# Kernel optimization log

Hardware: AMD Instinct MI355X
Metric: run time of the kernel (lower is better)

The kernel has to match this reference:

```python
import jax, jax.numpy as jnp
import numpy as np

N_HEADS = 16
N_KV_HEADS = 8
DIM = 2048
HEAD_DIM = DIM // N_HEADS  # 128
N_REP = N_HEADS // N_KV_HEADS


def _rope(t, cos, sin):
    # t: [B, S, H, D]; cos/sin: [S, D//2]
    t2 = t.reshape(*t.shape[:-1], -1, 2)  # [B,S,H,D/2,2]
    p1, p2 = t2[..., 0], t2[..., 1]
    c = cos[None, :, None, :]
    s = sin[None, :, None, :]
    r1 = p1 * c - p2 * s
    r2 = p1 * s + p2 * c
    return jnp.stack((r1, r2), axis=-1).reshape(t.shape)


def setup_inputs() -> dict:
    key = jax.random.key(0)
    ks = jax.random.split(key, 7)
    B, S = 2, 2048
    x = jax.random.normal(ks[0], (B, S, DIM), dtype=jnp.float32)
    freqs_cos = jax.random.normal(ks[1], (S, HEAD_DIM // 2), dtype=jnp.float32)
    freqs_sin = jax.random.normal(ks[2], (S, HEAD_DIM // 2), dtype=jnp.float32)
    sc = 1.0 / np.sqrt(DIM)
    wq = jax.random.normal(ks[3], (DIM, N_HEADS * HEAD_DIM), dtype=jnp.float32) * sc
    wk = jax.random.normal(ks[4], (DIM, N_KV_HEADS * HEAD_DIM), dtype=jnp.float32) * sc
    wv = jax.random.normal(ks[5], (DIM, N_KV_HEADS * HEAD_DIM), dtype=jnp.float32) * sc
    wo = jax.random.normal(ks[6], (N_HEADS * HEAD_DIM, DIM), dtype=jnp.float32) * sc
    return {"x": x, "freqs_cos": freqs_cos, "freqs_sin": freqs_sin,
            "wq": wq, "wk": wk, "wv": wv, "wo": wo}


def reference(x, freqs_cos, freqs_sin, wq, wk, wv, wo):
    B, S, _ = x.shape
    xq = (x @ wq).reshape(B, S, N_HEADS, HEAD_DIM)
    xk = (x @ wk).reshape(B, S, N_KV_HEADS, HEAD_DIM)
    xv = (x @ wv).reshape(B, S, N_KV_HEADS, HEAD_DIM)
    xq = _rope(xq, freqs_cos, freqs_sin)
    xk = _rope(xk, freqs_cos, freqs_sin)
    # GQA repeat_kv: [B,S,Hkv,D] -> [B,S,Hkv*n_rep,D]
    xk = jnp.repeat(xk, N_REP, axis=2)
    xv = jnp.repeat(xv, N_REP, axis=2)
    q = xq.transpose(0, 2, 1, 3)  # [B,H,S,D]
    k = xk.transpose(0, 2, 1, 3)
    v = xv.transpose(0, 2, 1, 3)
    scale = 1.0 / np.sqrt(HEAD_DIM)
    scores = jnp.einsum('bhqd,bhkd->bhqk', q, k) * scale
    causal = jnp.tril(jnp.ones((S, S), dtype=bool))
    scores = jnp.where(causal[None, None], scores, -jnp.inf)
    probs = jax.nn.softmax(scores.astype(jnp.float32), axis=-1).astype(q.dtype)
    out = jnp.einsum('bhqk,bhkd->bhqd', probs, v)
    out = out.transpose(0, 2, 1, 3).reshape(B, S, N_HEADS * HEAD_DIM)
    return out @ wo
```

## Files before the change

kernel.cpp:

```cpp
#include <hip/hip_runtime.h>
#include <cstdint>
#include <cstddef>

#define S_LEN 2048
#define DIM_   2048
#define NH   16
#define NKV  8
#define HD   128

typedef __attribute__((ext_vector_type(8))) __bf16 bf16x8;
typedef __attribute__((ext_vector_type(4))) float  f32x4;

typedef const __attribute__((address_space(1))) void* gptr_t;
typedef __attribute__((address_space(3))) void*       sptr_t;

static __device__ __forceinline__ float bf2f(unsigned short u) {
  union { unsigned int i; float f; } v; v.i = ((unsigned int)u) << 16; return v.f;
}
static __device__ __forceinline__ unsigned short f2bf(float f) {
  union { float f; unsigned int i; } v; v.f = f;
  unsigned int u = v.i;
  unsigned int r = (u + 0x7FFFu + ((u >> 16) & 1u)) >> 16;
  return (unsigned short)r;
}
static __device__ __forceinline__ unsigned int cvt_pk_bf16(float a, float b) {
  unsigned int r;
  asm volatile("v_cvt_pk_bf16_f32 %0, %1, %2" : "=v"(r) : "v"(a), "v"(b));
  return r;
}

#define QSCALE 0.12751744f
#define RESC_THR 11.542f

__global__ void k_prep(const float* __restrict__ x, unsigned short* __restrict__ xb,
                       const float* __restrict__ wq, const float* __restrict__ wk,
                       const float* __restrict__ wv, const float* __restrict__ wo,
                       unsigned short* __restrict__ wqkvT, unsigned short* __restrict__ woT) {
  int bid = blockIdx.x;
  if (bid < 8192) {
    int i = bid * 256 + threadIdx.x;
    float4 v = ((const float4*)x)[i];
    ushort4 o; o.x = f2bf(v.x); o.y = f2bf(v.y); o.z = f2bf(v.z); o.w = f2bf(v.w);
    ((ushort4*)xb)[i] = o;
    return;
  }
  bid -= 8192;
  const float* src; unsigned short* dst; int N, ntx;
  if (bid < 1024)      { src = wq; dst = wqkvT;                       N = 2048; ntx = 32; }
  else if (bid < 1536) { bid -= 1024; src = wk; dst = wqkvT + (size_t)2048 * 2048; N = 1024; ntx = 16; }
  else if (bid < 2048) { bid -= 1536; src = wv; dst = wqkvT + (size_t)3072 * 2048; N = 1024; ntx = 16; }
  else                 { bid -= 2048; src = wo; dst = woT;            N = 2048; ntx = 32; }
  const int K = 2048;
  __shared__ float tile[64][65];
  int lx = threadIdx.x & 15, ly = threadIdx.x >> 4;
  int r0 = (bid / ntx) * 64, c0 = (bid % ntx) * 64;
  #pragma unroll
  for (int i = 0; i < 4; i++) {
    int row = ly + 16 * i;
    float4 v = *(const float4*)(&src[(size_t)(r0 + row) * N + c0 + lx * 4]);
    tile[row][lx * 4 + 0] = v.x; tile[row][lx * 4 + 1] = v.y;
    tile[row][lx * 4 + 2] = v.z; tile[row][lx * 4 + 3] = v.w;
  }
  __syncthreads();
  #pragma unroll
  for (int i = 0; i < 4; i++) {
    int nrow = ly + 16 * i;
    ushort4 o;
    o.x = f2bf(tile[lx * 4 + 0][nrow]); o.y = f2bf(tile[lx * 4 + 1][nrow]);
    o.z = f2bf(tile[lx * 4 + 2][nrow]); o.w = f2bf(tile[lx * 4 + 3][nrow]);
    *(ushort4*)(&dst[(size_t)(c0 + nrow) * K + r0 + lx * 4]) = o;
  }
}

template<int MODE, int BM_, int TPB>
__global__ __launch_bounds__(TPB, 2) void k_gemm_bt(
    const unsigned short* __restrict__ A, const unsigned short* __restrict__ BT,
    void* __restrict__ C, int N, int K,
    const float* __restrict__ fc, const float* __restrict__ fs,
    unsigned short* __restrict__ kb, unsigned short* __restrict__ vb) {
  constexpr int NI = (BM_ == 64) ? 2 : 4;
  constexpr int AR = (BM_ * 64) / (TPB * 8);
  constexpr int BR = (128 * 64) / (TPB * 8);
  __shared__ __align__(16) unsigned short Asm[BM_ * 64];
  __shared__ __align__(16) unsigned short Bsm[128 * 64];
  const int t = threadIdx.x;
  const int lane = t & 63, w = t >> 6;
  const int wm = (BM_ == 64) ? 0 : (w >> 1) * 64;
  const int wn = (BM_ == 64) ? w * 32 : (w & 1) * 64;
  const int col = lane & 15, quad = lane >> 4;
  const int m0 = blockIdx.y * BM_, n0 = blockIdx.x * 128;

  f32x4 acc[4][NI];
  #pragma unroll
  for (int i = 0; i < 4; i++)
    #pragma unroll
    for (int j = 0; j < NI; j++) acc[i][j] = (f32x4){0.f, 0.f, 0.f, 0.f};

  for (int kk = 0; kk < K; kk += 64) {
    #pragma unroll
    for (int r = 0; r < AR; ++r) {
      int c = t + r * TPB;
      int c0 = (t & ~63) + r * TPB;
      int row = c >> 3;
      int kcs = (c & 7) ^ (row & 7);
      const unsigned short* gA = A + (size_t)(m0 + row) * K + kk + kcs * 8;
      __builtin_amdgcn_global_load_lds((gptr_t)gA, (sptr_t)(&Asm[c0 * 8]), 16, 0, 0);
    }
    #pragma unroll
    for (int r = 0; r < BR; ++r) {
      int c = t + r * TPB;
      int c0 = (t & ~63) + r * TPB;
      int row = c >> 3;
      int kcs = (c & 7) ^ (row & 7);
      const unsigned short* gB = BT + (size_t)(n0 + row) * K + kk + kcs * 8;
      __builtin_amdgcn_global_load_lds((gptr_t)gB, (sptr_t)(&Bsm[c0 * 8]), 16, 0, 0);
    }
    __syncthreads();
    #pragma unroll
    for (int kc2 = 0; kc2 < 2; kc2++) {
      bf16x8 af[4], bf[NI];
      #pragma unroll
      for (int mi = 0; mi < 4; mi++) {
        int rowA = wm + mi * 16 + col;
        af[mi] = *(const bf16x8*)(&Asm[rowA * 64 + (((kc2 * 4 + quad) ^ (col & 7)) * 8)]);
      }
      #pragma unroll
      for (int ni = 0; ni < NI; ni++) {
        int rowB = wn + ni * 16 + col;
        bf[ni] = *(const bf16x8*)(&Bsm[rowB * 64 + (((kc2 * 4 + quad) ^ (col & 7)) * 8)]);
      }
      #pragma unroll
      for (int mi = 0; mi < 4; mi++)
        #pragma unroll
        for (int ni = 0; ni < NI; ni++)
          acc[mi][ni] = __builtin_amdgcn_mfma_f32_16x16x32_bf16(af[mi], bf[ni], acc[mi][ni], 0, 0, 0);
    }
    __syncthreads();
  }

  #pragma unroll
  for (int mi = 0; mi < 4; mi++) {
    int row_base = m0 + wm + mi * 16 + quad * 4;
    #pragma unroll
    for (int ni = 0; ni < NI; ni++) {
      int col_g = n0 + wn + ni * 16 + col;
      if (MODE == 1) {
        float* O = (float*)C;
        #pragma unroll
        for (int r = 0; r < 4; r++) O[(size_t)(row_base + r) * N + col_g] = acc[mi][ni][r];
      } else {
        int region = col_g >> 10;
        if (region < 3) {
          int ri = (col_g & 127) >> 1;
          float sgn = (col_g & 1) ? 1.f : -1.f;
          unsigned short* qO = (unsigned short*)C;
          #pragma unroll
          for (int r = 0; r < 4; r++) {
            int row = row_base + r;
            int s = row & (S_LEN - 1);
            float cv = fc[s * 64 + ri], sv = fs[s * 64 + ri];
            float val = acc[mi][ni][r];
            float other = __shfl_xor(val, 1);
            float res = val * cv + sgn * other * sv;
            if (region < 2) qO[(size_t)row * 2048 + col_g] = f2bf(res * QSCALE);
            else            kb[(size_t)row * 1024 + (col_g - 2048)] = f2bf(res);
          }
        } else {
          int n_local = col_g - 3072;
          int b = row_base >> 11, s = row_base & (S_LEN - 1);
          int kvh = n_local >> 7, d = n_local & (HD - 1);
          ushort4 o4;
          o4.x = f2bf(acc[mi][ni][0]); o4.y = f2bf(acc[mi][ni][1]);
          o4.z = f2bf(acc[mi][ni][2]); o4.w = f2bf(acc[mi][ni][3]);
          *(ushort4*)(&vb[((size_t)((b * NKV + kvh) * HD + d)) * S_LEN + s]) = o4;
        }
      }
    }
  }
}

#define KLD 136
#define VLD 72
#define PLD 72
__global__ __launch_bounds__(512, 2) void k_attn(
    const unsigned short* __restrict__ q, const unsigned short* __restrict__ k,
    const unsigned short* __restrict__ vT, unsigned short* __restrict__ ao) {
  __shared__ __align__(16) unsigned short Ksm[64 * KLD];
  __shared__ __align__(16) unsigned short Vsm[128 * VLD];
  __shared__ __align__(16) unsigned short Psm[8 * 16 * PLD];
  const int t = threadIdx.x;
  const int lane = t & 63, w = t >> 6;
  const int col = lane & 15, quad = lane >> 4;
  const int g = blockIdx.x;
  const int b = g >> 3, kvh = g & 7;
  const int h = kvh * 2 + (w >> 2);
  const int yi = blockIdx.y;
  const int my_qt = (yi < 16) ? yi : 47 - yi;
  const int qrow = my_qt * 64 + (w & 3) * 16;
  unsigned short* Pw = &Psm[w * 16 * PLD];

  const int ki0 = t >> 4,        kdc = t & 15;
  const int ki1 = (t + 512) >> 4;
  const int vd0 = t >> 3,        vkc = t & 7;
  const int vd1 = (t + 512) >> 3;
  const unsigned short* kg0 = k + ((size_t)(b * S_LEN + ki0)) * (NKV * HD) + kvh * HD + kdc * 8;
  const unsigned short* kg1 = k + ((size_t)(b * S_LEN + ki1)) * (NKV * HD) + kvh * HD + kdc * 8;
  const unsigned short* vg0 = vT + ((size_t)((b * NKV + kvh) * HD + vd0)) * S_LEN + vkc * 8;
  const unsigned short* vg1 = vT + ((size_t)((b * NKV + kvh) * HD + vd1)) * S_LEN + vkc * 8;
  const size_t KSTEP = (size_t)64 * (NKV * HD);
  const size_t VSTEP = 64;

  bf16x8 qf[4];
  const size_t qbase = ((size_t)(b * S_LEN) + qrow + col) * DIM_ + h * HD;
  #pragma unroll
  for (int kc = 0; kc < 4; kc++) qf[kc] = *(const bf16x8*)(q + qbase + kc * 32 + quad * 8);

  f32x4 o[8];
  #pragma unroll
  for (int i = 0; i < 8; i++) o[i] = (f32x4){0.f, 0.f, 0.f, 0.f};
  float m_i = -1e30f;
  float l_i = 0.f;

  const int nkt = my_qt + 1;

  {
    uint4 kr0 = *(const uint4*)kg0;
    uint4 kr1 = *(const uint4*)kg1;
    uint4 vr0 = *(const uint4*)vg0;
    uint4 vr1 = *(const uint4*)vg1;
    *(uint4*)(&Ksm[ki0 * KLD + kdc * 8]) = kr0;
    *(uint4*)(&Ksm[ki1 * KLD + kdc * 8]) = kr1;
    *(uint4*)(&Vsm[vd0 * VLD + vkc * 8]) = vr0;
    *(uint4*)(&Vsm[vd1 * VLD + vkc * 8]) = vr1;
  }
  __syncthreads();

  for (int kt = 0; kt < nkt; ++kt) {
    const bool more = (kt + 1 < nkt);
    uint4 kr0, kr1, vr0, vr1;
    if (more) {
      kg0 += KSTEP; kg1 += KSTEP;
      kr0 = *(const uint4*)kg0;
      kr1 = *(const uint4*)kg1;
    }

    float p[4][4];
    __builtin_amdgcn_s_setprio(1);
    #pragma unroll
    for (int nt = 0; nt < 4; nt++) {
      f32x4 s_acc = (f32x4){0.f, 0.f, 0.f, 0.f};
      #pragma unroll
      for (int kc = 0; kc < 4; kc++) {
        bf16x8 kf = *(const bf16x8*)(&Ksm[(nt * 16 + col) * KLD + kc * 32 + quad * 8]);
        s_acc = __builtin_amdgcn_mfma_f32_16x16x32_bf16(kf, qf[kc], s_acc, 0, 0, 0);
      }
      #pragma unroll
      for (int r = 0; r < 4; r++) p[nt][r] = s_acc[r];
    }
    __builtin_amdgcn_s_setprio(0);

    if (kt == my_qt) {
      const int qglob = qrow + col;
      #pragma unroll
      for (int nt = 0; nt < 4; nt++)
        #pragma unroll
        for (int r = 0; r < 4; r++)
          if (kt * 64 + nt * 16 + quad * 4 + r > qglob) p[nt][r] = -1e30f;
    }

    float mx = fmaxf(fmaxf(fmaxf(p[0][0], p[0][1]), fmaxf(p[0][2], p[0][3])),
                     fmaxf(fmaxf(p[1][0], p[1][1]), fmaxf(p[1][2], p[1][3])));
    mx = fmaxf(mx, fmaxf(fmaxf(fmaxf(p[2][0], p[2][1]), fmaxf(p[2][2], p[2][3])),
                         fmaxf(fmaxf(p[3][0], p[3][1]), fmaxf(p[3][2], p[3][3]))));
    float mxs = fmaxf(mx, __shfl_xor(mx, 16));
    mxs = fmaxf(mxs, __shfl_xor(mxs, 32));
    float pe[4][4];
    #pragma unroll
    for (int nt = 0; nt < 4; nt++)
      #pragma unroll
      for (int r = 0; r < 4; r++) pe[nt][r] = exp2f(p[nt][r] - m_i);
    float rs = ((pe[0][0] + pe[0][1]) + (pe[0][2] + pe[0][3]))
             + ((pe[1][0] + pe[1][1]) + (pe[1][2] + pe[1][3]))
             + ((pe[2][0] + pe[2][1]) + (pe[2][2] + pe[2][3]))
             + ((pe[3][0] + pe[3][1]) + (pe[3][2] + pe[3][3]));
    if (__any(mxs - m_i > RESC_THR)) {
      float mn = fmaxf(m_i, mxs);
      float alpha = exp2f(m_i - mn);
      m_i = mn; l_i *= alpha;
      float ar[4];
      #pragma unroll
      for (int r = 0; r < 4; r++) ar[r] = __shfl(alpha, quad * 4 + r);
      #pragma unroll
      for (int dt = 0; dt < 8; dt++)
        #pragma unroll
        for (int r = 0; r < 4; r++) o[dt][r] *= ar[r];
      #pragma unroll
      for (int nt = 0; nt < 4; nt++)
        #pragma unroll
        for (int r = 0; r < 4; r++) pe[nt][r] = exp2f(p[nt][r] - m_i);
      rs = ((pe[0][0] + pe[0][1]) + (pe[0][2] + pe[0][3]))
         + ((pe[1][0] + pe[1][1]) + (pe[1][2] + pe[1][3]))
         + ((pe[2][0] + pe[2][1]) + (pe[2][2] + pe[2][3]))
         + ((pe[3][0] + pe[3][1]) + (pe[3][2] + pe[3][3]));
    }
    rs += __shfl_xor(rs, 16);
    rs += __shfl_xor(rs, 32);
    l_i += rs;

    #pragma unroll
    for (int nt = 0; nt < 4; nt++) {
      uint2 pk;
      pk.x = cvt_pk_bf16(pe[nt][0], pe[nt][1]);
      pk.y = cvt_pk_bf16(pe[nt][2], pe[nt][3]);
      *(uint2*)(&Pw[col * PLD + nt * 16 + quad * 4]) = pk;
    }

    __syncthreads();

    if (more) {
      *(uint4*)(&Ksm[ki0 * KLD + kdc * 8]) = kr0;
      *(uint4*)(&Ksm[ki1 * KLD + kdc * 8]) = kr1;
      vg0 += VSTEP; vg1 += VSTEP;
      vr0 = *(const uint4*)vg0;
      vr1 = *(const uint4*)vg1;
    }

    bf16x8 pf[2];
    #pragma unroll
    for (int kc2 = 0; kc2 < 2; kc2++)
      pf[kc2] = *(const bf16x8*)(&Pw[col * PLD + kc2 * 32 + quad * 8]);

    __builtin_amdgcn_s_setprio(1);
    #pragma unroll
    for (int dt = 0; dt < 8; dt++) {
      #pragma unroll
      for (int kc2 = 0; kc2 < 2; kc2++) {
        bf16x8 vf = *(const bf16x8*)(&Vsm[(dt * 16 + col) * VLD + kc2 * 32 + quad * 8]);
        o[dt] = __builtin_amdgcn_mfma_f32_16x16x32_bf16(pf[kc2], vf, o[dt], 0, 0, 0);
      }
    }
    __builtin_amdgcn_s_setprio(0);

    __syncthreads();

    if (more) {
      *(uint4*)(&Vsm[vd0 * VLD + vkc * 8]) = vr0;
      *(uint4*)(&Vsm[vd1 * VLD + vkc * 8]) = vr1;
    }
  }

  float linv[4];
  #pragma unroll
  for (int r = 0; r < 4; r++) linv[r] = 1.f / __shfl(l_i, quad * 4 + r);
  #pragma unroll
  for (int dt = 0; dt < 8; dt++) {
    int dcol = h * HD + dt * 16 + col;
    #pragma unroll
    for (int r = 0; r < 4; r++) {
      int rg = qrow + quad * 4 + r;
      ao[((size_t)(b * S_LEN) + rg) * DIM_ + dcol] = f2bf(o[dt][r] * linv[r]);
    }
  }
}

extern "C" void kernel_launch(void* const* d_in, const int* in_sizes, int n_in,
                              void* d_out, int out_size, void* d_ws, size_t ws_size,
                              hipStream_t stream) {
  const float* x  = (const float*)d_in[0];
  const float* fc = (const float*)d_in[1];
  const float* fs = (const float*)d_in[2];
  const float* wq = (const float*)d_in[3];
  const float* wk = (const float*)d_in[4];
  const float* wv = (const float*)d_in[5];
  const float* wo = (const float*)d_in[6];
  float* out = (float*)d_out;

  char* ws = (char*)d_ws;
  const size_t MB = 1024 * 1024;
  unsigned short* xb    = (unsigned short*)(ws + 0 * MB);
  unsigned short* wqkvT = (unsigned short*)(ws + 16 * MB);
  unsigned short* woT   = (unsigned short*)(ws + 32 * MB);
  unsigned short* qb    = (unsigned short*)(ws + 40 * MB);
  unsigned short* kb    = (unsigned short*)(ws + 56 * MB);
  unsigned short* vT    = (unsigned short*)(ws + 64 * MB);
  unsigned short* ao    = (unsigned short*)(ws + 72 * MB);

  k_prep<<<dim3(11264), dim3(256), 0, stream>>>(x, xb, wq, wk, wv, wo, wqkvT, woT);
  k_gemm_bt<3, 128, 256><<<dim3(32, 32), dim3(256), 0, stream>>>(xb, wqkvT, (void*)qb, 4096, 2048, fc, fs, kb, vT);
  k_attn<<<dim3(16, 32), dim3(512), 0, stream>>>(qb, kb, vT, ao);
  k_gemm_bt<1, 64, 256><<<dim3(16, 64), dim3(256), 0, stream>>>(ao, woT, (void*)out, 2048, 2048, nullptr, nullptr, nullptr, nullptr);
}
```

Measured before the change: 322.9 us.

## Split attention blocks per head instead of sharing K/V across GQA head pair

The attention kernel now launches one 256-thread block per (batch, head, query tile) instead of 512-thread blocks that covered both query heads of a KV group. The query-tile order becomes a simple longest-first reverse mapping in place of the paired balancing scheme. Each thread now loads four K and four V chunks per tile, and V prefetch moves to the start of the iteration. This gives more, smaller blocks for better occupancy and scheduling, at the cost of loading each K/V tile twice, once per head sharing it, and higher register pressure from the larger prefetch buffers.

Measured after the change: 433.9 us. 34.3% more time.

```diff
diff --git a/kernel.cpp b/kernel.cpp
--- a/kernel.cpp
+++ b/kernel.cpp
@@ -182,31 +182,28 @@
 #define KLD 136
 #define VLD 72
 #define PLD 72
-__global__ __launch_bounds__(512, 2) void k_attn(
+__global__ __launch_bounds__(256, 3) void k_attn(
     const unsigned short* __restrict__ q, const unsigned short* __restrict__ k,
     const unsigned short* __restrict__ vT, unsigned short* __restrict__ ao) {
   __shared__ __align__(16) unsigned short Ksm[64 * KLD];
   __shared__ __align__(16) unsigned short Vsm[128 * VLD];
-  __shared__ __align__(16) unsigned short Psm[8 * 16 * PLD];
+  __shared__ __align__(16) unsigned short Psm[4 * 16 * PLD];
   const int t = threadIdx.x;
   const int lane = t & 63, w = t >> 6;
   const int col = lane & 15, quad = lane >> 4;
-  const int g = blockIdx.x;
-  const int b = g >> 3, kvh = g & 7;
-  const int h = kvh * 2 + (w >> 2);
-  const int yi = blockIdx.y;
-  const int my_qt = (yi < 16) ? yi : 47 - yi;
-  const int qrow = my_qt * 64 + (w & 3) * 16;
+  const int bh = blockIdx.x;
+  const int b = bh >> 4, h = bh & 15;
+  const int kvh = h >> 1;
+  const int my_qt = 31 - blockIdx.y;
+  const int qrow = my_qt * 64 + w * 16;
   unsigned short* Pw = &Psm[w * 16 * PLD];
 
-  const int ki0 = t >> 4,        kdc = t & 15;
-  const int ki1 = (t + 512) >> 4;
-  const int vd0 = t >> 3,        vkc = t & 7;
-  const int vd1 = (t + 512) >> 3;
-  const unsigned short* kg0 = k + ((size_t)(b * S_LEN + ki0)) * (NKV * HD) + kvh * HD + kdc * 8;
-  const unsigned short* kg1 = k + ((size_t)(b * S_LEN + ki1)) * (NKV * HD) + kvh * HD + kdc * 8;
-  const unsigned short* vg0 = vT + ((size_t)((b * NKV + kvh) * HD + vd0)) * S_LEN + vkc * 8;
-  const unsigned short* vg1 = vT + ((size_t)((b * NKV + kvh) * HD + vd1)) * S_LEN + vkc * 8;
+  const int ki = t >> 4, kdc = t & 15;
+  const int vd = t >> 3, vkc = t & 7;
+  const unsigned short* kg = k + ((size_t)(b * S_LEN + ki)) * (NKV * HD) + kvh * HD + kdc * 8;
+  const unsigned short* vg = vT + ((size_t)((b * NKV + kvh) * HD + vd)) * S_LEN + vkc * 8;
+  const size_t KROW = (size_t)16 * (NKV * HD);
+  const size_t VROW = (size_t)32 * S_LEN;
   const size_t KSTEP = (size_t)64 * (NKV * HD);
   const size_t VSTEP = 64;
 
@@ -224,24 +221,26 @@
   const int nkt = my_qt + 1;
 
   {
-    uint4 kr0 = *(const uint4*)kg0;
-    uint4 kr1 = *(const uint4*)kg1;
-    uint4 vr0 = *(const uint4*)vg0;
-    uint4 vr1 = *(const uint4*)vg1;
-    *(uint4*)(&Ksm[ki0 * KLD + kdc * 8]) = kr0;
-    *(uint4*)(&Ksm[ki1 * KLD + kdc * 8]) = kr1;
-    *(uint4*)(&Vsm[vd0 * VLD + vkc * 8]) = vr0;
-    *(uint4*)(&Vsm[vd1 * VLD + vkc * 8]) = vr1;
+    #pragma unroll
+    for (int cc = 0; cc < 4; cc++) {
+      uint4 kr = *(const uint4*)(kg + cc * KROW);
+      *(uint4*)(&Ksm[(ki + cc * 16) * KLD + kdc * 8]) = kr;
+      uint4 vr = *(const uint4*)(vg + cc * VROW);
+      *(uint4*)(&Vsm[(vd + cc * 32) * VLD + vkc * 8]) = vr;
+    }
   }
   __syncthreads();
 
   for (int kt = 0; kt < nkt; ++kt) {
     const bool more = (kt + 1 < nkt);
-    uint4 kr0, kr1, vr0, vr1;
+    uint4 kr[4], vr[4];
     if (more) {
-      kg0 += KSTEP; kg1 += KSTEP;
-      kr0 = *(const uint4*)kg0;
-      kr1 = *(const uint4*)kg1;
+      kg += KSTEP; vg += VSTEP;
+      #pragma unroll
+      for (int cc = 0; cc < 4; cc++) {
+        kr[cc] = *(const uint4*)(kg + cc * KROW);
+        vr[cc] = *(const uint4*)(vg + cc * VROW);
+      }
     }
 
     float p[4][4];
@@ -318,11 +317,9 @@
     __syncthreads();
 
     if (more) {
-      *(uint4*)(&Ksm[ki0 * KLD + kdc * 8]) = kr0;
-      *(uint4*)(&Ksm[ki1 * KLD + kdc * 8]) = kr1;
-      vg0 += VSTEP; vg1 += VSTEP;
-      vr0 = *(const uint4*)vg0;
-      vr1 = *(const uint4*)vg1;
+      #pragma unroll
+      for (int cc = 0; cc < 4; cc++)
+        *(uint4*)(&Ksm[(ki + cc * 16) * KLD + kdc * 8]) = kr[cc];
     }
 
     bf16x8 pf[2];
@@ -344,8 +341,9 @@
     __syncthreads();
 
     if (more) {
-      *(uint4*)(&Vsm[vd0 * VLD + vkc * 8]) = vr0;
-      *(uint4*)(&Vsm[vd1 * VLD + vkc * 8]) = vr1;
+      #pragma unroll
+      for (int cc = 0; cc < 4; cc++)
+        *(uint4*)(&Vsm[(vd + cc * 32) * VLD + vkc * 8]) = vr[cc];
     }
   }
 
@@ -387,6 +385,6 @@
 
   k_prep<<<dim3(11264), dim3(256), 0, stream>>>(x, xb, wq, wk, wv, wo, wqkvT, woT);
   k_gemm_bt<3, 128, 256><<<dim3(32, 32), dim3(256), 0, stream>>>(xb, wqkvT, (void*)qb, 4096, 2048, fc, fs, kb, vT);
-  k_attn<<<dim3(16, 32), dim3(512), 0, stream>>>(qb, kb, vT, ao);
+  k_attn<<<dim3(32, 32), dim3(256), 0, stream>>>(qb, kb, vT, ao);
   k_gemm_bt<1, 64, 256><<<dim3(16, 64), dim3(256), 0, stream>>>(ao, woT, (void*)out, 2048, 2048, nullptr, nullptr, nullptr, nullptr);
 }
```
